# Performance work log

Measured on AMD Instinct MI355X. Metric: run time of the kernel, lower is better.

## Reference

```python
import jax, jax.numpy as jnp
import numpy as np
import math

LIMBS = [(5, 7), (7, 9), (6, 8), (8, 10), (11, 13), (13, 15), (12, 14), (14, 16), (5, 6), (11, 12), (5, 11), (6, 12), (5, 12), (6, 11)]
PARENT = jnp.array([l[0] for l in LIMBS], dtype=jnp.int32)
CHILD = jnp.array([l[1] for l in LIMBS], dtype=jnp.int32)
EXPECTED_2D_LEN = 0.15

B = 65536
D_MODEL = 64
HID = 128


def _ln(x, g, b, eps=1e-5):
    m = jnp.mean(x, axis=-1, keepdims=True)
    v = jnp.mean(jnp.square(x - m), axis=-1, keepdims=True)
    return (x - m) * jax.lax.rsqrt(v + eps) * g + b


def _unit(x, eps=1e-6):
    # F.normalize semantics: divide by max(norm, eps)
    n = jnp.linalg.norm(x, axis=-1, keepdims=True)
    return x / jnp.maximum(n, eps)


def setup_inputs() -> dict:
    key = jax.random.key(0)
    ks = jax.random.split(key, 32)
    d = {}
    d["joint_features"] = jax.random.normal(ks[0], (B, 17, D_MODEL), jnp.float32)
    d["pose_2d"] = jax.random.normal(ks[1], (B, 17, 2), jnp.float32)
    d["pose_3d"] = jax.random.normal(ks[2], (B, 17, 3), jnp.float32)
    d["azimuth"] = jax.random.uniform(ks[3], (B,), jnp.float32) * 360.0
    d["elevation"] = jax.random.uniform(ks[4], (B,), jnp.float32) * 180.0 - 90.0
    d["projected_2d"] = jax.random.normal(ks[5], (B, 17, 2), jnp.float32)

    def lin(k, out_f, in_f, std=None):
        s = std if std is not None else 1.0 / math.sqrt(in_f)
        return jax.random.normal(k, (out_f, in_f), jnp.float32) * s

    # current_orient_encoder: Linear(3->32), LayerNorm(32), ReLU
    d["co_w"] = lin(ks[6], HID // 4, 3)
    d["co_b"] = jnp.zeros((HID // 4,), jnp.float32)
    d["co_g"] = jnp.ones((HID // 4,), jnp.float32)
    d["co_be"] = jnp.zeros((HID // 4,), jnp.float32)
    # limb_2d_encoder: Linear(4->64), LayerNorm(64), ReLU
    d["l2_w"] = lin(ks[7], HID // 2, 4)
    d["l2_b"] = jnp.zeros((HID // 2,), jnp.float32)
    d["l2_g"] = jnp.ones((HID // 2,), jnp.float32)
    d["l2_be"] = jnp.zeros((HID // 2,), jnp.float32)
    # view_encoder: Linear(7->32), ReLU
    d["v_w"] = lin(ks[8], HID // 4, 7)
    d["v_b"] = jnp.zeros((HID // 4,), jnp.float32)
    # limb_head: Linear(256->128), LN(128), LeakyReLU, Linear(128->128), LeakyReLU, Linear(128->3)
    in_dim = HID // 2 + HID // 4 + D_MODEL * 2 + HID // 4  # 256
    d["h1_w"] = lin(ks[9], HID, in_dim)
    d["h1_b"] = jnp.zeros((HID,), jnp.float32)
    d["h_g"] = jnp.ones((HID,), jnp.float32)
    d["h_be"] = jnp.zeros((HID,), jnp.float32)
    d["h2_w"] = lin(ks[10], HID, HID)
    d["h2_b"] = jnp.zeros((HID,), jnp.float32)
    d["h3_w"] = lin(ks[11], 3, HID, std=0.01)
    d["h3_b"] = jnp.zeros((3,), jnp.float32)
    return d


def reference(joint_features, pose_2d, pose_3d, azimuth, elevation, projected_2d,
              co_w, co_b, co_g, co_be, l2_w, l2_b, l2_g, l2_be, v_w, v_b,
              h1_w, h1_b, h_g, h_be, h2_w, h2_b, h3_w, h3_b):
    nl = PARENT.shape[0]  # 14
    # gather parent/child joint features: (B, 14, d_model)
    pf = joint_features[:, PARENT, :]
    cf = joint_features[:, CHILD, :]
    # current 3D orientations from input pose
    cur = _unit(pose_3d[:, CHILD, :] - pose_3d[:, PARENT, :])  # (B,14,3)
    co = jax.nn.relu(_ln(jnp.einsum('blk,ok->blo', cur, co_w) + co_b, co_g, co_be))
    # view encoder from azimuth/elevation
    az = azimuth * (math.pi / 180.0)
    el = elevation * (math.pi / 180.0)
    sa, ca, se, ce = jnp.sin(az), jnp.cos(az), jnp.sin(el), jnp.cos(el)
    view_in = jnp.stack([sa * ce, se, ca * ce, sa, ca, se, ce], axis=-1)  # (B,7)
    vf = jax.nn.relu(view_in @ v_w.T + v_b)  # (B,32)
    vf = jnp.broadcast_to(vf[:, None, :], (vf.shape[0], nl, vf.shape[-1]))
    # 2D foreshortening features from projected_2d
    v2 = projected_2d[:, CHILD, :] - projected_2d[:, PARENT, :]  # (B,14,2)
    L = jnp.linalg.norm(v2, axis=-1, keepdims=True)
    d2 = v2 / (L + 1e-6)
    ratio = L / (EXPECTED_2D_LEN + 1e-6)
    feat2d = jnp.concatenate([d2, L, ratio], axis=-1)  # (B,14,4)
    l2 = jax.nn.relu(_ln(jnp.einsum('blk,ok->blo', feat2d, l2_w) + l2_b, l2_g, l2_be))
    # concat all branches: (B,14,256)
    lf = jnp.concatenate([l2, co, pf, cf, vf], axis=-1)
    # 3-layer MLP head
    h = jax.nn.leaky_relu(_ln(jnp.einsum('blk,ok->blo', lf, h1_w) + h1_b, h_g, h_be), 0.2)
    h = jax.nn.leaky_relu(jnp.einsum('blk,ok->blo', h, h2_w) + h2_b, 0.2)
    delta = jnp.einsum('blk,ok->blo', h, h3_w) + h3_b  # (B,14,3)
    return _unit(cur + delta)
```

## Files before the change

kernel.cpp:

```cpp
#include <hip/hip_runtime.h>


#define NTHR   1024
#define NBLK   256
#define NTILES 14336
#define NROWS  917504
#define C2D    6.66662222251852f
#define RAD    0.017453292519943295f
#define WS_STAT_OFF 98304
#define WS_SCAL_OFF 131072

typedef __bf16 bf16x8 __attribute__((ext_vector_type(8)));
typedef __bf16 bf16x4 __attribute__((ext_vector_type(4)));
typedef float  f32x4  __attribute__((ext_vector_type(4)));

#define PARENT_PK 0x10106097863120ull
#define CHILD_PK  0x677671b9a85342ull

__global__ __launch_bounds__(256) void prep_kernel(
    const float* __restrict__ w1, const float* __restrict__ w2,
    __bf16* __restrict__ wsb)
{
  const int u = blockIdx.x * 256 + threadIdx.x;
  if (u < 4096) {
    const int lane = u & 63, t = u >> 6;
    const int f = t & 1, kk = (t >> 1) & 7, wn = t >> 4;
    const int col = wn * 32 + f * 16 + (lane & 15);
    const int kb  = kk * 32 + (lane >> 4) * 8;
    __bf16* dst = wsb + (size_t)u * 8;
    #pragma unroll
    for (int j = 0; j < 8; ++j) dst[j] = (__bf16)w1[col * 256 + kb + j];
  } else if (u < 6144) {
    const int v = u - 4096;
    const int lane = v & 63, t = v >> 6;
    const int f = t & 1, kk = (t >> 1) & 3, wn = t >> 3;
    const int col = wn * 32 + f * 16 + (lane & 15);
    const int kb  = kk * 32 + (lane >> 4) * 8;
    __bf16* dst = wsb + 32768 + (size_t)v * 8;
    #pragma unroll
    for (int j = 0; j < 8; ++j) dst[j] = (__bf16)w2[col * 128 + kb + j];
  }
}

__global__ __launch_bounds__(64) void prep0_kernel(
    const float* __restrict__ cow, const float* __restrict__ cob,
    const float* __restrict__ l2w, const float* __restrict__ l2b,
    float* __restrict__ statg)
{
  const int o = threadIdx.x;
  const float w0 = l2w[o * 4 + 0], w1v = l2w[o * 4 + 1];
  const float w2v = l2w[o * 4 + 2] + C2D * l2w[o * 4 + 3];
  const float bo = l2b[o];
  float v[14] = { w0, w1v, w2v, bo, w0 * w0, w0 * w1v, w0 * w2v,
                  w1v * w1v, w1v * w2v, w2v * w2v, w0 * bo, w1v * bo, w2v * bo, bo * bo };
  float c0 = 0.f, c1 = 0.f, c2 = 0.f, cb = 0.f;
  if (o < 32) { c0 = cow[o * 3 + 0]; c1 = cow[o * 3 + 1]; c2 = cow[o * 3 + 2]; cb = cob[o]; }
  float u[14] = { c0, c1, c2, cb, c0 * c0, c0 * c1, c0 * c2,
                  c1 * c1, c1 * c2, c2 * c2, c0 * cb, c1 * cb, c2 * cb, cb * cb };
  #pragma unroll
  for (int k = 0; k < 14; ++k) {
    #pragma unroll
    for (int m = 1; m < 64; m <<= 1) { v[k] += __shfl_xor(v[k], m, 64); u[k] += __shfl_xor(u[k], m, 64); }
  }
  if (o == 0) {
    const float i64 = 1.f / 64.f, i32 = 1.f / 32.f;
    const float lmx = v[0] * i64, lmy = v[1] * i64, lmz = v[2] * i64, lmb = v[3] * i64;
    statg[0] = lmx; statg[1] = lmy; statg[2] = lmz; statg[3] = lmb;
    statg[4] = v[4] * i64 - lmx * lmx;        statg[5] = 2.f * (v[5] * i64 - lmx * lmy);
    statg[6] = 2.f * (v[6] * i64 - lmx * lmz); statg[7] = v[7] * i64 - lmy * lmy;
    statg[8] = 2.f * (v[8] * i64 - lmy * lmz); statg[9] = v[9] * i64 - lmz * lmz;
    statg[10] = 2.f * (v[10] * i64 - lmx * lmb); statg[11] = 2.f * (v[11] * i64 - lmy * lmb);
    statg[12] = 2.f * (v[12] * i64 - lmz * lmb); statg[13] = v[13] * i64 - lmb * lmb;
    const float cmx = u[0] * i32, cmy = u[1] * i32, cmz = u[2] * i32, cmb = u[3] * i32;
    statg[14] = cmx; statg[15] = cmy; statg[16] = cmz; statg[17] = cmb;
    statg[18] = u[4] * i32 - cmx * cmx;        statg[19] = 2.f * (u[5] * i32 - cmx * cmy);
    statg[20] = 2.f * (u[6] * i32 - cmx * cmz); statg[21] = u[7] * i32 - cmy * cmy;
    statg[22] = 2.f * (u[8] * i32 - cmy * cmz); statg[23] = u[9] * i32 - cmz * cmz;
    statg[24] = 2.f * (u[10] * i32 - cmx * cmb); statg[25] = 2.f * (u[11] * i32 - cmy * cmb);
    statg[26] = 2.f * (u[12] * i32 - cmz * cmb); statg[27] = u[13] * i32 - cmb * cmb;
  }
}

__global__ __launch_bounds__(256) void prep2_kernel(
    const float* __restrict__ p3g, const float* __restrict__ az,
    const float* __restrict__ el,  const float* __restrict__ p2d,
    const float* __restrict__ statg, f32x4* __restrict__ scalg)
{
  const int r = blockIdx.x * 256 + threadIdx.x;
  const unsigned rg = (unsigned)r;
  const unsigned b = rg / 14u;
  const int l = (int)(rg - b * 14u);
  const int p = 5 + (int)((PARENT_PK >> (4 * l)) & 15ull);
  const int c = 5 + (int)((CHILD_PK  >> (4 * l)) & 15ull);
  const float* p3 = p3g + (size_t)b * 51;
  const float dx = p3[c * 3 + 0] - p3[p * 3 + 0];
  const float dy = p3[c * 3 + 1] - p3[p * 3 + 1];
  const float dz = p3[c * 3 + 2] - p3[p * 3 + 2];
  const float* q2 = p2d + (size_t)b * 34;
  const float vx = q2[c * 2 + 0] - q2[p * 2 + 0];
  const float vy = q2[c * 2 + 1] - q2[p * 2 + 1];
  const float sazv = az[b], selv = el[b];

  const float ci = 1.f / fmaxf(sqrtf(dx * dx + dy * dy + dz * dz), 1e-6f);
  const float cx = dx * ci, cy = dy * ci, cz = dz * ci;
  const float L  = sqrtf(vx * vx + vy * vy);
  const float il = 1.f / (L + 1e-6f);
  const float f0 = vx * il, f1 = vy * il;
  const float azr = sazv * RAD, elr = selv * RAD;
  const float sa = __sinf(azr), ca = __cosf(azr);
  const float se = __sinf(elr), ce = __cosf(elr);
  const float vl = statg[4] * f0 * f0 + statg[7] * f1 * f1 + statg[9] * L * L +
                   statg[5] * f0 * f1 + statg[6] * f0 * L + statg[8] * f1 * L +
                   statg[10] * f0 + statg[11] * f1 + statg[12] * L + statg[13];
  const float vc = statg[18] * cx * cx + statg[21] * cy * cy + statg[23] * cz * cz +
                   statg[19] * cx * cy + statg[20] * cx * cz + statg[22] * cy * cz +
                   statg[24] * cx + statg[25] * cy + statg[26] * cz + statg[27];
  f32x4 s0; s0[0] = cx; s0[1] = cy; s0[2] = cz; s0[3] = f0;
  f32x4 s1; s1[0] = f1; s1[1] = L; s1[2] = rsqrtf(vl + 1e-5f); s1[3] = rsqrtf(vc + 1e-5f);
  f32x4 s2; s2[0] = sa * ce; s2[1] = se; s2[2] = ca * ce; s2[3] = sa;
  f32x4 s3; s3[0] = ca; s3[1] = ce; s3[2] = 0.f; s3[3] = 0.f;
  scalg[(size_t)r * 4 + 0] = s0; scalg[(size_t)r * 4 + 1] = s1;
  scalg[(size_t)r * 4 + 2] = s2; scalg[(size_t)r * 4 + 3] = s3;
}

struct Smem {
  __bf16 w1f[32768];
  __bf16 w2f[16384];
  __bf16 lf[64][264];
  __bf16 h [64][132];
  f32x4  scal4[256];
  float  w3c[384];
  float  h1b[128], hg[128], hbe[128], h2b[128];
  float  partG1[512];
  float  partG2[768];
};

__device__ __forceinline__ float RFL(float x) {
  return __uint_as_float((unsigned)__builtin_amdgcn_readfirstlane((int)__float_as_uint(x)));
}

template<bool PRECOMP>
__global__ __launch_bounds__(NTHR, 4) void limb_kernel(
    const float* __restrict__ jf,  const float* __restrict__ p3g,
    const float* __restrict__ az,  const float* __restrict__ el,
    const float* __restrict__ p2d,
    const float* __restrict__ cow, const float* __restrict__ cob,
    const float* __restrict__ cog, const float* __restrict__ cobe,
    const float* __restrict__ l2w, const float* __restrict__ l2b,
    const float* __restrict__ l2g, const float* __restrict__ l2be,
    const float* __restrict__ vw,  const float* __restrict__ vb,
    const float* __restrict__ h1bg, const float* __restrict__ hgg,
    const float* __restrict__ hbeg, const float* __restrict__ h2bg,
    const float* __restrict__ w3,  const float* __restrict__ h3bg,
    const __bf16* __restrict__ wsb, const f32x4* __restrict__ scalg,
    float* __restrict__ out)
{
  __shared__ Smem sm;
  const int tid  = threadIdx.x;
  const int wave = tid >> 6;
  const int lane = tid & 63;
  const int lrow = lane & 15, lk8 = lane >> 4;
  const int mp = wave >> 2, nt = wave & 3;
  const int nrow = nt * 16 + lrow;
  const int cb0 = mp * 32 + lk8 * 4;
  const int cb1 = cb0 + 16;
  const int myrow0 = wave * 4;

  {
    const uint4* s1 = (const uint4*)wsb;
    uint4* d1 = (uint4*)sm.w1f;
    for (int i = tid; i < 4096; i += NTHR) d1[i] = s1[i];
    const uint4* s2 = (const uint4*)(wsb + 32768);
    uint4* d2 = (uint4*)sm.w2f;
    for (int i = tid; i < 2048; i += NTHR) d2[i] = s2[i];
  }
  if (tid < 384) sm.w3c[tid] = w3[tid];
  if (tid < 128) {
    sm.h1b[tid] = h1bg[tid]; sm.hg[tid] = hgg[tid];
    sm.hbe[tid] = hbeg[tid]; sm.h2b[tid] = h2bg[tid];
  }
  const float h3b0 = h3bg[0], h3b1 = h3bg[1], h3b2 = h3bg[2];

  float lQxx, lQxy2, lQxz2, lQyy, lQyz2, lQzz, lrx2, lry2, lrz2, ls0;
  float lmx, lmy, lmz, lmb;
  {
    float s1x = 0, s1y = 0, s1z = 0, sb = 0;
    float sxx = 0, sxy = 0, sxz = 0, syy = 0, syz = 0, szz = 0;
    float sbx = 0, sby = 0, sbz = 0, sbb = 0;
    for (int o = 0; o < 64; ++o) {
      const float w0 = l2w[o * 4 + 0], w1v = l2w[o * 4 + 1];
      const float w2v = l2w[o * 4 + 2] + C2D * l2w[o * 4 + 3];
      const float bo = l2b[o];
      s1x += w0; s1y += w1v; s1z += w2v; sb += bo;
      sxx += w0 * w0; sxy += w0 * w1v; sxz += w0 * w2v;
      syy += w1v * w1v; syz += w1v * w2v; szz += w2v * w2v;
      sbx += w0 * bo; sby += w1v * bo; sbz += w2v * bo; sbb += bo * bo;
    }
    const float i = 1.f / 64.f;
    lmx = RFL(s1x * i); lmy = RFL(s1y * i); lmz = RFL(s1z * i); lmb = RFL(sb * i);
    lQxx = RFL(sxx * i - lmx * lmx); lQxy2 = RFL(2.f * (sxy * i - lmx * lmy));
    lQxz2 = RFL(2.f * (sxz * i - lmx * lmz)); lQyy = RFL(syy * i - lmy * lmy);
    lQyz2 = RFL(2.f * (syz * i - lmy * lmz)); lQzz = RFL(szz * i - lmz * lmz);
    lrx2 = RFL(2.f * (sbx * i - lmx * lmb)); lry2 = RFL(2.f * (sby * i - lmy * lmb));
    lrz2 = RFL(2.f * (sbz * i - lmz * lmb)); ls0 = RFL(sbb * i - lmb * lmb);
  }
  float cQxx, cQxy2, cQxz2, cQyy, cQyz2, cQzz, crx2, cry2, crz2, cs0;
  float cmx, cmy, cmz, cmb;
  {
    float s1x = 0, s1y = 0, s1z = 0, sb = 0;
    float sxx = 0, sxy = 0, sxz = 0, syy = 0, syz = 0, szz = 0;
    float sbx = 0, sby = 0, sbz = 0, sbb = 0;
    for (int o = 0; o < 32; ++o) {
      const float w0 = cow[o * 3 + 0], w1v = cow[o * 3 + 1], w2v = cow[o * 3 + 2];
      const float bo = cob[o];
      s1x += w0; s1y += w1v; s1z += w2v; sb += bo;
      sxx += w0 * w0; sxy += w0 * w1v; sxz += w0 * w2v;
      syy += w1v * w1v; syz += w1v * w2v; szz += w2v * w2v;
      sbx += w0 * bo; sby += w1v * bo; sbz += w2v * bo; sbb += bo * bo;
    }
    const float i = 1.f / 32.f;
    cmx = RFL(s1x * i); cmy = RFL(s1y * i); cmz = RFL(s1z * i); cmb = RFL(sb * i);
    cQxx = RFL(sxx * i - cmx * cmx); cQxy2 = RFL(2.f * (sxy * i - cmx * cmy));
    cQxz2 = RFL(2.f * (sxz * i - cmx * cmz)); cQyy = RFL(syy * i - cmy * cmy);
    cQyz2 = RFL(2.f * (syz * i - cmy * cmz)); cQzz = RFL(szz * i - cmz * cmz);
    crx2 = RFL(2.f * (sbx * i - cmx * cmb)); cry2 = RFL(2.f * (sby * i - cmy * cmb));
    crz2 = RFL(2.f * (sbz * i - cmz * cmb)); cs0 = RFL(sbb * i - cmb * cmb);
  }

  const float lwc0 = l2w[lane * 4 + 0] - lmx;
  const float lwc1 = l2w[lane * 4 + 1] - lmy;
  const float lwc2 = (l2w[lane * 4 + 2] + C2D * l2w[lane * 4 + 3]) - lmz;
  const float lbc  = l2b[lane] - lmb;
  const float lgv  = l2g[lane], lbev = l2be[lane];
  float u0, u1, u2, u3, u4, u5, u6;
  if (lane < 32) {
    u0 = cow[lane * 3 + 0] - cmx; u1 = cow[lane * 3 + 1] - cmy;
    u2 = cow[lane * 3 + 2] - cmz; u3 = cob[lane] - cmb;
    u4 = cog[lane]; u5 = cobe[lane]; u6 = 0.f;
  } else {
    const int o = lane - 32;
    u0 = vw[o * 7 + 0]; u1 = vw[o * 7 + 1] + vw[o * 7 + 5];
    u2 = vw[o * 7 + 2]; u3 = vw[o * 7 + 3];
    u4 = vw[o * 7 + 4]; u5 = vw[o * 7 + 6]; u6 = vb[o];
  }

  auto jf_src = [&](int rg0x, int round) -> const float* {
    const int task = wave * 8 + round * 4 + lk8;
    const int row = task >> 1, half = task & 1;
    const unsigned rg = (unsigned)(rg0x + row);
    const unsigned b = rg / 14u;
    const int l = (int)(rg - b * 14u);
    const int j = half ? 5 + (int)((CHILD_PK >> (4 * l)) & 15ull)
                       : 5 + (int)((PARENT_PK >> (4 * l)) & 15ull);
    return jf + ((size_t)b * 17 + (size_t)j) * 64 + lrow * 4;
  };
  auto jf_store = [&](int round, float4 v) {
    const int task = wave * 8 + round * 4 + lk8;
    const int row = task >> 1, half = task & 1;
    bf16x4 o; o[0] = (__bf16)v.x; o[1] = (__bf16)v.y; o[2] = (__bf16)v.z; o[3] = (__bf16)v.w;
    *(bf16x4*)&sm.lf[row][(half ? 160 : 96) + lrow * 4] = o;
  };
  struct G12 { float p3p0, p3p1, p3p2, p3c0, p3c1, p3c2, q2p0, q2p1, q2c0, q2c1, sazv, selv; };
  auto gather12_row = [&](int rgl) -> G12 {
    G12 g;
    const unsigned rg = (unsigned)rgl;
    const unsigned b = rg / 14u;
    const int l = (int)(rg - b * 14u);
    const int p = 5 + (int)((PARENT_PK >> (4 * l)) & 15ull);
    const int c = 5 + (int)((CHILD_PK  >> (4 * l)) & 15ull);
    const float* p3 = p3g + (size_t)b * 51;
    g.p3p0 = p3[p * 3 + 0]; g.p3p1 = p3[p * 3 + 1]; g.p3p2 = p3[p * 3 + 2];
    g.p3c0 = p3[c * 3 + 0]; g.p3c1 = p3[c * 3 + 1]; g.p3c2 = p3[c * 3 + 2];
    const float* q2 = p2d + (size_t)b * 34;
    g.q2p0 = q2[p * 2 + 0]; g.q2p1 = q2[p * 2 + 1];
    g.q2c0 = q2[c * 2 + 0]; g.q2c1 = q2[c * 2 + 1];
    g.sazv = az[b]; g.selv = el[b];
    return g;
  };
  auto scal_write = [&](int row, const G12& g) {
    const float dx = g.p3c0 - g.p3p0, dy = g.p3c1 - g.p3p1, dz = g.p3c2 - g.p3p2;
    const float ci = 1.f / fmaxf(sqrtf(dx * dx + dy * dy + dz * dz), 1e-6f);
    const float cx = dx * ci, cy = dy * ci, cz = dz * ci;
    const float vx = g.q2c0 - g.q2p0, vy = g.q2c1 - g.q2p1;
    const float L  = sqrtf(vx * vx + vy * vy);
    const float il = 1.f / (L + 1e-6f);
    const float f0 = vx * il, f1 = vy * il;
    const float azr = g.sazv * RAD, elr = g.selv * RAD;
    const float sa = __sinf(azr), ca = __cosf(azr);
    const float se = __sinf(elr), ce = __cosf(elr);
    const float vl = lQxx * f0 * f0 + lQyy * f1 * f1 + lQzz * L * L +
                     lQxy2 * f0 * f1 + lQxz2 * f0 * L + lQyz2 * f1 * L +
                     lrx2 * f0 + lry2 * f1 + lrz2 * L + ls0;
    const float vc = cQxx * cx * cx + cQyy * cy * cy + cQzz * cz * cz +
                     cQxy2 * cx * cy + cQxz2 * cx * cz + cQyz2 * cy * cz +
                     crx2 * cx + cry2 * cy + crz2 * cz + cs0;
    f32x4 s0; s0[0] = cx; s0[1] = cy; s0[2] = cz; s0[3] = f0;
    f32x4 s1; s1[0] = f1; s1[1] = L; s1[2] = rsqrtf(vl + 1e-5f); s1[3] = rsqrtf(vc + 1e-5f);
    f32x4 s2; s2[0] = sa * ce; s2[1] = se; s2[2] = ca * ce; s2[3] = sa;
    f32x4 s3; s3[0] = ca; s3[1] = ce; s3[2] = 0.f; s3[3] = 0.f;
    sm.scal4[row * 4 + 0] = s0; sm.scal4[row * 4 + 1] = s1;
    sm.scal4[row * 4 + 2] = s2; sm.scal4[row * 4 + 3] = s3;
  };
  auto expandB = [&]() {
    #pragma unroll
    for (int rr = 0; rr < 4; ++rr) {
      const int row = myrow0 + rr;
      const f32x4 s0 = sm.scal4[row * 4 + 0];
      const f32x4 s1 = sm.scal4[row * 4 + 1];
      const f32x4 s2 = sm.scal4[row * 4 + 2];
      const f32x4 s3 = sm.scal4[row * 4 + 3];
      {
        const float a = lwc0 * s0[3] + lwc1 * s1[0] + lwc2 * s1[1] + lbc;
        sm.lf[row][lane] = (__bf16)fmaxf(a * s1[2] * lgv + lbev, 0.f);
      }
      if (lane < 32) {
        const float a = u0 * s0[0] + u1 * s0[1] + u2 * s0[2] + u3;
        sm.lf[row][64 + lane] = (__bf16)fmaxf(a * s1[3] * u4 + u5, 0.f);
      } else {
        const float a = u0 * s2[0] + u1 * s2[1] + u2 * s2[2] + u3 * s2[3] +
                        u4 * s3[0] + u5 * s3[1] + u6;
        sm.lf[row][224 + (lane - 32)] = (__bf16)fmaxf(a, 0.f);
      }
    }
  };

  {
    const int rg0 = blockIdx.x * 64;
    jf_store(0, *(const float4*)jf_src(rg0, 0));
    jf_store(1, *(const float4*)jf_src(rg0, 1));
    if (PRECOMP) {
      if (lane < 16)
        sm.scal4[(myrow0 + (lane >> 2)) * 4 + (lane & 3)] =
            scalg[(size_t)(rg0 + myrow0 + (lane >> 2)) * 4 + (lane & 3)];
    } else if (lane < 4) {
      scal_write(myrow0 + lane, gather12_row(rg0 + myrow0 + lane));
    }
    expandB();
  }
  __syncthreads();

  float curx = 0.f, cury = 0.f, curz = 0.f;
  int prevT = -1;

  for (int tile = blockIdx.x; tile < NTILES; tile += NBLK) {
    const int ntile = tile + NBLK;
    const bool pv = ntile < NTILES;

    float4 jva = {0.f, 0.f, 0.f, 0.f}, jvb = jva;
    f32x4 sn = {0.f, 0.f, 0.f, 0.f};
    G12 g = {};
    if (pv) {
      jva = *(const float4*)jf_src(ntile * 64, 0);
      jvb = *(const float4*)jf_src(ntile * 64, 1);
      if (PRECOMP) {
        if (lane < 16)
          sn = scalg[(size_t)(ntile * 64 + myrow0 + (lane >> 2)) * 4 + (lane & 3)];
      } else if (lane < 4) {
        g = gather12_row(ntile * 64 + myrow0 + lane);
      }
    }
    if (prevT >= 0 && lane < 4) {
      const int r = myrow0 + lane;
      const f32x4 q0 = *(const f32x4*)&sm.partG2[r * 12];
      const f32x4 q1 = *(const f32x4*)&sm.partG2[r * 12 + 4];
      const f32x4 q2 = *(const f32x4*)&sm.partG2[r * 12 + 8];
      const float ox = curx + q0[0] + q0[1] + q0[2] + q0[3] + h3b0;
      const float oy = cury + q1[0] + q1[1] + q1[2] + q1[3] + h3b1;
      const float oz = curz + q2[0] + q2[1] + q2[2] + q2[3] + h3b2;
      const float nn = sqrtf(ox * ox + oy * oy + oz * oz);
      const float iv = 1.f / fmaxf(nn, 1e-6f);
      const size_t o0 = (size_t)(prevT * 64 + r) * 3;
      out[o0 + 0] = ox * iv; out[o0 + 1] = oy * iv; out[o0 + 2] = oz * iv;
    }
    f32x4 a0 = {0.f, 0.f, 0.f, 0.f}, a1 = a0;
    #pragma unroll
    for (int kk = 0; kk < 8; ++kk) {
      const bf16x8 fb  = *(const bf16x8*)&sm.lf[nrow][kk * 32 + lk8 * 8];
      const bf16x8 fa0 = *(const bf16x8*)&sm.w1f[(((mp * 8 + kk) * 2 + 0) * 64 + lane) * 8];
      const bf16x8 fa1 = *(const bf16x8*)&sm.w1f[(((mp * 8 + kk) * 2 + 1) * 64 + lane) * 8];
      a0 = __builtin_amdgcn_mfma_f32_16x16x32_bf16(fa0, fb, a0, 0, 0, 0);
      a1 = __builtin_amdgcn_mfma_f32_16x16x32_bf16(fa1, fb, a1, 0, 0, 0);
    }
    const f32x4 hb0 = *(const f32x4*)&sm.h1b[cb0];
    const f32x4 hb1 = *(const f32x4*)&sm.h1b[cb1];
    float v0[4], v1[4], ss = 0.f, qq = 0.f;
    #pragma unroll
    for (int j = 0; j < 4; ++j) {
      v0[j] = a0[j] + hb0[j]; v1[j] = a1[j] + hb1[j];
      ss += v0[j] + v1[j];
      qq = fmaf(v0[j], v0[j], qq); qq = fmaf(v1[j], v1[j], qq);
    }
    ss += __shfl_xor(ss, 16, 64); ss += __shfl_xor(ss, 32, 64);
    qq += __shfl_xor(qq, 16, 64); qq += __shfl_xor(qq, 32, 64);
    if (lk8 == 0) *(float2*)&sm.partG1[nrow * 8 + mp * 2] = make_float2(ss, qq);
    __syncthreads();

    {
      const f32x4 pa = *(const f32x4*)&sm.partG1[nrow * 8];
      const f32x4 pb = *(const f32x4*)&sm.partG1[nrow * 8 + 4];
      const float mean = (pa[0] + pa[2] + pb[0] + pb[2]) * (1.f / 128.f);
      const float var  = (pa[1] + pa[3] + pb[1] + pb[3]) * (1.f / 128.f) - mean * mean;
      const float rs = rsqrtf(var + 1e-5f);
      const f32x4 g0 = *(const f32x4*)&sm.hg[cb0],  g1 = *(const f32x4*)&sm.hg[cb1];
      const f32x4 e0 = *(const f32x4*)&sm.hbe[cb0], e1 = *(const f32x4*)&sm.hbe[cb1];
      bf16x4 y0, y1;
      #pragma unroll
      for (int j = 0; j < 4; ++j) {
        float t0 = (v0[j] - mean) * rs * g0[j] + e0[j]; t0 = (t0 > 0.f) ? t0 : 0.2f * t0;
        float t1 = (v1[j] - mean) * rs * g1[j] + e1[j]; t1 = (t1 > 0.f) ? t1 : 0.2f * t1;
        y0[j] = (__bf16)t0; y1[j] = (__bf16)t1;
      }
      *(bf16x4*)&sm.h[nrow][cb0] = y0;
      *(bf16x4*)&sm.h[nrow][cb1] = y1;
    }
    __syncthreads();

    f32x4 d0 = {0.f, 0.f, 0.f, 0.f}, d1 = d0;
    #pragma unroll
    for (int kk = 0; kk < 4; ++kk) {
      const bf16x8 fbh = *(const bf16x8*)&sm.h[nrow][kk * 32 + lk8 * 8];
      const bf16x8 fa0 = *(const bf16x8*)&sm.w2f[(((mp * 4 + kk) * 2 + 0) * 64 + lane) * 8];
      const bf16x8 fa1 = *(const bf16x8*)&sm.w2f[(((mp * 4 + kk) * 2 + 1) * 64 + lane) * 8];
      d0 = __builtin_amdgcn_mfma_f32_16x16x32_bf16(fa0, fbh, d0, 0, 0, 0);
      d1 = __builtin_amdgcn_mfma_f32_16x16x32_bf16(fa1, fbh, d1, 0, 0, 0);
    }
    if (pv) { jf_store(0, jva); jf_store(1, jvb); }
    if (lane < 4) {
      const f32x4 cu = sm.scal4[(myrow0 + lane) * 4];
      curx = cu[0]; cury = cu[1]; curz = cu[2];
    }
    if (pv) {
      if (PRECOMP) {
        if (lane < 16)
          sm.scal4[(myrow0 + (lane >> 2)) * 4 + (lane & 3)] = sn;
      } else if (lane < 4) {
        scal_write(myrow0 + lane, g);
      }
    }
    {
      const f32x4 b20 = *(const f32x4*)&sm.h2b[cb0], b21 = *(const f32x4*)&sm.h2b[cb1];
      const f32x4 wx0 = *(const f32x4*)&sm.w3c[cb0],        wx1 = *(const f32x4*)&sm.w3c[cb1];
      const f32x4 wy0 = *(const f32x4*)&sm.w3c[128 + cb0],  wy1 = *(const f32x4*)&sm.w3c[128 + cb1];
      const f32x4 wz0 = *(const f32x4*)&sm.w3c[256 + cb0],  wz1 = *(const f32x4*)&sm.w3c[256 + cb1];
      float p0 = 0.f, p1 = 0.f, p2 = 0.f;
      #pragma unroll
      for (int j = 0; j < 4; ++j) {
        float x0 = d0[j] + b20[j]; x0 = (x0 > 0.f) ? x0 : 0.2f * x0;
        float x1 = d1[j] + b21[j]; x1 = (x1 > 0.f) ? x1 : 0.2f * x1;
        p0 = fmaf(x0, wx0[j], fmaf(x1, wx1[j], p0));
        p1 = fmaf(x0, wy0[j], fmaf(x1, wy1[j], p1));
        p2 = fmaf(x0, wz0[j], fmaf(x1, wz1[j], p2));
      }
      p0 += __shfl_xor(p0, 16, 64); p0 += __shfl_xor(p0, 32, 64);
      p1 += __shfl_xor(p1, 16, 64); p1 += __shfl_xor(p1, 32, 64);
      p2 += __shfl_xor(p2, 16, 64); p2 += __shfl_xor(p2, 32, 64);
      if (lk8 == 0) {
        sm.partG2[nrow * 12 + 0 + mp] = p0;
        sm.partG2[nrow * 12 + 4 + mp] = p1;
        sm.partG2[nrow * 12 + 8 + mp] = p2;
      }
    }
    if (pv) expandB();
    __syncthreads();
    prevT = tile;
  }

  if (lane < 4) {
    const int r = myrow0 + lane;
    const f32x4 q0 = *(const f32x4*)&sm.partG2[r * 12];
    const f32x4 q1 = *(const f32x4*)&sm.partG2[r * 12 + 4];
    const f32x4 q2 = *(const f32x4*)&sm.partG2[r * 12 + 8];
    const float ox = curx + q0[0] + q0[1] + q0[2] + q0[3] + h3b0;
    const float oy = cury + q1[0] + q1[1] + q1[2] + q1[3] + h3b1;
    const float oz = curz + q2[0] + q2[1] + q2[2] + q2[3] + h3b2;
    const float nn = sqrtf(ox * ox + oy * oy + oz * oz);
    const float iv = 1.f / fmaxf(nn, 1e-6f);
    const size_t o0 = (size_t)(prevT * 64 + r) * 3;
    out[o0 + 0] = ox * iv; out[o0 + 1] = oy * iv; out[o0 + 2] = oz * iv;
  }
}

extern "C" void kernel_launch(void* const* d_in, const int* in_sizes, int n_in,
                              void* d_out, int out_size, void* d_ws, size_t ws_size,
                              hipStream_t stream) {
  (void)in_sizes; (void)n_in; (void)out_size;
  const float* jf   = (const float*)d_in[0];
  const float* p3   = (const float*)d_in[2];
  const float* az   = (const float*)d_in[3];
  const float* el   = (const float*)d_in[4];
  const float* p2d  = (const float*)d_in[5];
  const float* cow  = (const float*)d_in[6];
  const float* cob  = (const float*)d_in[7];
  const float* cog  = (const float*)d_in[8];
  const float* cobe = (const float*)d_in[9];
  const float* l2w  = (const float*)d_in[10];
  const float* l2b  = (const float*)d_in[11];
  const float* l2g  = (const float*)d_in[12];
  const float* l2be = (const float*)d_in[13];
  const float* vw   = (const float*)d_in[14];
  const float* vb   = (const float*)d_in[15];
  const float* w1   = (const float*)d_in[16];
  const float* h1b  = (const float*)d_in[17];
  const float* hg   = (const float*)d_in[18];
  const float* hbe  = (const float*)d_in[19];
  const float* w2   = (const float*)d_in[20];
  const float* h2b  = (const float*)d_in[21];
  const float* w3   = (const float*)d_in[22];
  const float* h3b  = (const float*)d_in[23];

  __bf16* wsb   = (__bf16*)d_ws;
  float*  statg = (float*)((char*)d_ws + WS_STAT_OFF);
  f32x4*  scalg = (f32x4*)((char*)d_ws + WS_SCAL_OFF);

  const size_t ws_need = (size_t)WS_SCAL_OFF + (size_t)NROWS * 64;
  const bool pre = ws_size >= ws_need;

  prep_kernel<<<dim3(24), dim3(256), 0, stream>>>(w1, w2, wsb);
  if (pre) {
    prep0_kernel<<<dim3(1), dim3(64), 0, stream>>>(cow, cob, l2w, l2b, statg);
    prep2_kernel<<<dim3(NROWS / 256), dim3(256), 0, stream>>>(p3, az, el, p2d, statg, scalg);
    limb_kernel<true><<<dim3(NBLK), dim3(NTHR), 0, stream>>>(
        jf, p3, az, el, p2d, cow, cob, cog, cobe,
        l2w, l2b, l2g, l2be, vw, vb,
        h1b, hg, hbe, h2b, w3, h3b, wsb, scalg, (float*)d_out);
  } else {
    limb_kernel<false><<<dim3(NBLK), dim3(NTHR), 0, stream>>>(
        jf, p3, az, el, p2d, cow, cob, cog, cobe,
        l2w, l2b, l2g, l2be, vw, vb,
        h1b, hg, hbe, h2b, w3, h3b, wsb, scalg, (float*)d_out);
  }
}
```

Before: 292.1 us.

## Compute small encoder branches with an MFMA over precomputed bf16 scalar features

The prep kernel now folds the LayerNorm statistics, gains and biases of the limb_2d, orientation and view encoders into a single 16-wide bf16 weight matrix. Each row's scalars are written as a 16-element bf16 feature vector plus a separate fp32 current-orientation buffer, instead of 64 bytes of fp32 scalars. In the main kernel the per-lane scalar expansion is replaced by two 16x16x32 MFMAs per wave. The lf concat layout and w1 columns are permuted so these branches occupy contiguous columns 0-127. This cuts per-row global traffic and VALU work in the expansion, at the cost of bf16 rounding of the normalized pre-activations and an extra barrier in the prologue.

```diff
diff --git a/kernel.cpp b/kernel.cpp
--- a/kernel.cpp
+++ b/kernel.cpp
@@ -7,8 +7,10 @@
 #define NROWS  917504
 #define C2D    6.66662222251852f
 #define RAD    0.017453292519943295f
-#define WS_STAT_OFF 98304
-#define WS_SCAL_OFF 131072
+#define WS_WSM_OFF  98304
+#define WS_STAT_OFF 106496
+#define WS_X_OFF    131072
+#define WS_CUR_OFF  (131072 + 29360128)
 
 typedef __bf16 bf16x8 __attribute__((ext_vector_type(8)));
 typedef __bf16 bf16x4 __attribute__((ext_vector_type(4)));
@@ -29,7 +31,11 @@
     const int kb  = kk * 32 + (lane >> 4) * 8;
     __bf16* dst = wsb + (size_t)u * 8;
     #pragma unroll
-    for (int j = 0; j < 8; ++j) dst[j] = (__bf16)w1[col * 256 + kb + j];
+    for (int j = 0; j < 8; ++j) {
+      const int kn = kb + j;
+      const int ko = kn < 96 ? kn : (kn < 128 ? kn + 128 : kn - 32);
+      dst[j] = (__bf16)w1[col * 256 + ko];
+    }
   } else if (u < 6144) {
     const int v = u - 4096;
     const int lane = v & 63, t = v >> 6;
@@ -42,19 +48,23 @@
   }
 }
 
-__global__ __launch_bounds__(64) void prep0_kernel(
+__global__ __launch_bounds__(128) void prep0_kernel(
     const float* __restrict__ cow, const float* __restrict__ cob,
+    const float* __restrict__ cog, const float* __restrict__ cobe,
     const float* __restrict__ l2w, const float* __restrict__ l2b,
-    float* __restrict__ statg)
+    const float* __restrict__ l2g, const float* __restrict__ l2be,
+    const float* __restrict__ vw,  const float* __restrict__ vb,
+    float* __restrict__ statg, __bf16* __restrict__ wsmg)
 {
-  const int o = threadIdx.x;
-  const float w0 = l2w[o * 4 + 0], w1v = l2w[o * 4 + 1];
-  const float w2v = l2w[o * 4 + 2] + C2D * l2w[o * 4 + 3];
-  const float bo = l2b[o];
+  const int tid = threadIdx.x;
+  const int o64 = tid & 63;
+  const float w0 = l2w[o64 * 4 + 0], w1v = l2w[o64 * 4 + 1];
+  const float w2v = l2w[o64 * 4 + 2] + C2D * l2w[o64 * 4 + 3];
+  const float bo = l2b[o64];
   float v[14] = { w0, w1v, w2v, bo, w0 * w0, w0 * w1v, w0 * w2v,
                   w1v * w1v, w1v * w2v, w2v * w2v, w0 * bo, w1v * bo, w2v * bo, bo * bo };
   float c0 = 0.f, c1 = 0.f, c2 = 0.f, cb = 0.f;
-  if (o < 32) { c0 = cow[o * 3 + 0]; c1 = cow[o * 3 + 1]; c2 = cow[o * 3 + 2]; cb = cob[o]; }
+  if (o64 < 32) { c0 = cow[o64 * 3 + 0]; c1 = cow[o64 * 3 + 1]; c2 = cow[o64 * 3 + 2]; cb = cob[o64]; }
   float u[14] = { c0, c1, c2, cb, c0 * c0, c0 * c1, c0 * c2,
                   c1 * c1, c1 * c2, c2 * c2, c0 * cb, c1 * cb, c2 * cb, cb * cb };
   #pragma unroll
@@ -62,16 +72,16 @@
     #pragma unroll
     for (int m = 1; m < 64; m <<= 1) { v[k] += __shfl_xor(v[k], m, 64); u[k] += __shfl_xor(u[k], m, 64); }
   }
-  if (o == 0) {
-    const float i64 = 1.f / 64.f, i32 = 1.f / 32.f;
-    const float lmx = v[0] * i64, lmy = v[1] * i64, lmz = v[2] * i64, lmb = v[3] * i64;
+  const float i64 = 1.f / 64.f, i32 = 1.f / 32.f;
+  const float lmx = v[0] * i64, lmy = v[1] * i64, lmz = v[2] * i64, lmb = v[3] * i64;
+  const float cmx = u[0] * i32, cmy = u[1] * i32, cmz = u[2] * i32, cmb = u[3] * i32;
+  if (tid == 0) {
     statg[0] = lmx; statg[1] = lmy; statg[2] = lmz; statg[3] = lmb;
     statg[4] = v[4] * i64 - lmx * lmx;        statg[5] = 2.f * (v[5] * i64 - lmx * lmy);
     statg[6] = 2.f * (v[6] * i64 - lmx * lmz); statg[7] = v[7] * i64 - lmy * lmy;
     statg[8] = 2.f * (v[8] * i64 - lmy * lmz); statg[9] = v[9] * i64 - lmz * lmz;
     statg[10] = 2.f * (v[10] * i64 - lmx * lmb); statg[11] = 2.f * (v[11] * i64 - lmy * lmb);
     statg[12] = 2.f * (v[12] * i64 - lmz * lmb); statg[13] = v[13] * i64 - lmb * lmb;
-    const float cmx = u[0] * i32, cmy = u[1] * i32, cmz = u[2] * i32, cmb = u[3] * i32;
     statg[14] = cmx; statg[15] = cmy; statg[16] = cmz; statg[17] = cmb;
     statg[18] = u[4] * i32 - cmx * cmx;        statg[19] = 2.f * (u[5] * i32 - cmx * cmy);
     statg[20] = 2.f * (u[6] * i32 - cmx * cmz); statg[21] = u[7] * i32 - cmy * cmy;
@@ -79,12 +89,52 @@
     statg[24] = 2.f * (u[10] * i32 - cmx * cmb); statg[25] = 2.f * (u[11] * i32 - cmy * cmb);
     statg[26] = 2.f * (u[12] * i32 - cmz * cmb); statg[27] = u[13] * i32 - cmb * cmb;
   }
+  float W[16];
+  #pragma unroll
+  for (int k = 0; k < 16; ++k) W[k] = 0.f;
+  const int col = tid;
+  if (col < 64) {
+    const float g = l2g[col], be = l2be[col];
+    W[0] = g * (l2w[col * 4 + 0] - lmx);
+    W[1] = g * (l2w[col * 4 + 1] - lmy);
+    W[2] = g * ((l2w[col * 4 + 2] + C2D * l2w[col * 4 + 3]) - lmz);
+    W[3] = g * (l2b[col] - lmb);
+    W[14] = be;
+  } else if (col < 96) {
+    const int o = col - 64;
+    const float g = cog[o], be = cobe[o];
+    W[4] = g * (cow[o * 3 + 0] - cmx);
+    W[5] = g * (cow[o * 3 + 1] - cmy);
+    W[6] = g * (cow[o * 3 + 2] - cmz);
+    W[7] = g * (cob[o] - cmb);
+    W[14] = be;
+  } else {
+    const int o = col - 96;
+    W[8]  = vw[o * 7 + 0];
+    W[9]  = vw[o * 7 + 1] + vw[o * 7 + 5];
+    W[10] = vw[o * 7 + 2];
+    W[11] = vw[o * 7 + 3];
+    W[12] = vw[o * 7 + 4];
+    W[13] = vw[o * 7 + 6];
+    W[14] = vb[o];
+  }
+  const int mp = col >> 5, f = (col >> 4) & 1, lcol = col & 15;
+  #pragma unroll
+  for (int kq = 0; kq < 4; ++kq) {
+    #pragma unroll
+    for (int j = 0; j < 8; ++j) {
+      const int k = kq * 8 + j;
+      wsmg[(size_t)(((mp * 2 + f) * 64 + kq * 16 + lcol)) * 8 + j] =
+          (__bf16)(k < 16 ? W[k] : 0.f);
+    }
+  }
 }
 
 __global__ __launch_bounds__(256) void prep2_kernel(
     const float* __restrict__ p3g, const float* __restrict__ az,
     const float* __restrict__ el,  const float* __restrict__ p2d,
-    const float* __restrict__ statg, f32x4* __restrict__ scalg)
+    const float* __restrict__ statg, __bf16* __restrict__ Xg,
+    f32x4* __restrict__ curg)
 {
   const int r = blockIdx.x * 256 + threadIdx.x;
   const unsigned rg = (unsigned)r;
@@ -115,12 +165,23 @@
   const float vc = statg[18] * cx * cx + statg[21] * cy * cy + statg[23] * cz * cz +
                    statg[19] * cx * cy + statg[20] * cx * cz + statg[22] * cy * cz +
                    statg[24] * cx + statg[25] * cy + statg[26] * cz + statg[27];
-  f32x4 s0; s0[0] = cx; s0[1] = cy; s0[2] = cz; s0[3] = f0;
-  f32x4 s1; s1[0] = f1; s1[1] = L; s1[2] = rsqrtf(vl + 1e-5f); s1[3] = rsqrtf(vc + 1e-5f);
-  f32x4 s2; s2[0] = sa * ce; s2[1] = se; s2[2] = ca * ce; s2[3] = sa;
-  f32x4 s3; s3[0] = ca; s3[1] = ce; s3[2] = 0.f; s3[3] = 0.f;
-  scalg[(size_t)r * 4 + 0] = s0; scalg[(size_t)r * 4 + 1] = s1;
-  scalg[(size_t)r * 4 + 2] = s2; scalg[(size_t)r * 4 + 3] = s3;
+  const float rs2 = rsqrtf(vl + 1e-5f);
+  const float rsc = rsqrtf(vc + 1e-5f);
+
+  __bf16 xr[16];
+  xr[0] = (__bf16)(f0 * rs2);  xr[1] = (__bf16)(f1 * rs2);
+  xr[2] = (__bf16)(L * rs2);   xr[3] = (__bf16)rs2;
+  xr[4] = (__bf16)(cx * rsc);  xr[5] = (__bf16)(cy * rsc);
+  xr[6] = (__bf16)(cz * rsc);  xr[7] = (__bf16)rsc;
+  xr[8] = (__bf16)(sa * ce);   xr[9] = (__bf16)se;
+  xr[10] = (__bf16)(ca * ce);  xr[11] = (__bf16)sa;
+  xr[12] = (__bf16)ca;         xr[13] = (__bf16)ce;
+  xr[14] = (__bf16)1.0f;       xr[15] = (__bf16)0.0f;
+  uint4* xd = (uint4*)(Xg + (size_t)r * 16);
+  xd[0] = *(const uint4*)&xr[0];
+  xd[1] = *(const uint4*)&xr[8];
+  f32x4 cu; cu[0] = cx; cu[1] = cy; cu[2] = cz; cu[3] = 0.f;
+  curg[r] = cu;
 }
 
 struct Smem {
@@ -128,7 +189,7 @@
   __bf16 w2f[16384];
   __bf16 lf[64][264];
   __bf16 h [64][132];
-  f32x4  scal4[256];
+  __bf16 X [64][40];
   float  w3c[384];
   float  h1b[128], hg[128], hbe[128], h2b[128];
   float  partG1[512];
@@ -152,7 +213,8 @@
     const float* __restrict__ h1bg, const float* __restrict__ hgg,
     const float* __restrict__ hbeg, const float* __restrict__ h2bg,
     const float* __restrict__ w3,  const float* __restrict__ h3bg,
-    const __bf16* __restrict__ wsb, const f32x4* __restrict__ scalg,
+    const __bf16* __restrict__ wsb, const __bf16* __restrict__ Xg,
+    const f32x4* __restrict__ curg,
     float* __restrict__ out)
 {
   __shared__ Smem sm;
@@ -166,6 +228,8 @@
   const int cb1 = cb0 + 16;
   const int myrow0 = wave * 4;
 
+  const bf16x8* __restrict__ wsm8 = (const bf16x8*)(wsb + 49152);
+
   {
     const uint4* s1 = (const uint4*)wsb;
     uint4* d1 = (uint4*)sm.w1f;
@@ -174,6 +238,7 @@
     uint4* d2 = (uint4*)sm.w2f;
     for (int i = tid; i < 2048; i += NTHR) d2[i] = s2[i];
   }
+  for (int i = tid; i < 64 * 40; i += NTHR) ((__bf16*)sm.X)[i] = (__bf16)0.0f;
   if (tid < 384) sm.w3c[tid] = w3[tid];
   if (tid < 128) {
     sm.h1b[tid] = h1bg[tid]; sm.hg[tid] = hgg[tid];
@@ -244,6 +309,8 @@
     u4 = vw[o * 7 + 4]; u5 = vw[o * 7 + 6]; u6 = vb[o];
   }
 
+  f32x4* const scal4u = (f32x4*)&sm.X[0][0];
+
   auto jf_src = [&](int rg0x, int round) -> const float* {
     const int task = wave * 8 + round * 4 + lk8;
     const int row = task >> 1, half = task & 1;
@@ -258,7 +325,7 @@
     const int task = wave * 8 + round * 4 + lk8;
     const int row = task >> 1, half = task & 1;
     bf16x4 o; o[0] = (__bf16)v.x; o[1] = (__bf16)v.y; o[2] = (__bf16)v.z; o[3] = (__bf16)v.w;
-    *(bf16x4*)&sm.lf[row][(half ? 160 : 96) + lrow * 4] = o;
+    *(bf16x4*)&sm.lf[row][(half ? 192 : 128) + lrow * 4] = o;
   };
   struct G12 { float p3p0, p3p1, p3p2, p3c0, p3c1, p3c2, q2p0, q2p1, q2c0, q2c1, sazv, selv; };
   auto gather12_row = [&](int rgl) -> G12 {
@@ -298,17 +365,17 @@
     f32x4 s1; s1[0] = f1; s1[1] = L; s1[2] = rsqrtf(vl + 1e-5f); s1[3] = rsqrtf(vc + 1e-5f);
     f32x4 s2; s2[0] = sa * ce; s2[1] = se; s2[2] = ca * ce; s2[3] = sa;
     f32x4 s3; s3[0] = ca; s3[1] = ce; s3[2] = 0.f; s3[3] = 0.f;
-    sm.scal4[row * 4 + 0] = s0; sm.scal4[row * 4 + 1] = s1;
-    sm.scal4[row * 4 + 2] = s2; sm.scal4[row * 4 + 3] = s3;
+    scal4u[row * 4 + 0] = s0; scal4u[row * 4 + 1] = s1;
+    scal4u[row * 4 + 2] = s2; scal4u[row * 4 + 3] = s3;
   };
   auto expandB = [&]() {
     #pragma unroll
     for (int rr = 0; rr < 4; ++rr) {
       const int row = myrow0 + rr;
-      const f32x4 s0 = sm.scal4[row * 4 + 0];
-      const f32x4 s1 = sm.scal4[row * 4 + 1];
-      const f32x4 s2 = sm.scal4[row * 4 + 2];
-      const f32x4 s3 = sm.scal4[row * 4 + 3];
+      const f32x4 s0 = scal4u[row * 4 + 0];
+      const f32x4 s1 = scal4u[row * 4 + 1];
+      const f32x4 s2 = scal4u[row * 4 + 2];
+      const f32x4 s3 = scal4u[row * 4 + 3];
       {
         const float a = lwc0 * s0[3] + lwc1 * s1[0] + lwc2 * s1[1] + lbc;
         sm.lf[row][lane] = (__bf16)fmaxf(a * s1[2] * lgv + lbev, 0.f);
@@ -319,9 +386,25 @@
       } else {
         const float a = u0 * s2[0] + u1 * s2[1] + u2 * s2[2] + u3 * s2[3] +
                         u4 * s3[0] + u5 * s3[1] + u6;
-        sm.lf[row][224 + (lane - 32)] = (__bf16)fmaxf(a, 0.f);
-      }
-    }
+        sm.lf[row][96 + (lane - 32)] = (__bf16)fmaxf(a, 0.f);
+      }
+    }
+  };
+  auto expandMFMA = [&]() {
+    const bf16x8 fbX = *(const bf16x8*)&sm.X[nrow][lk8 * 8];
+    const bf16x8 wa0 = wsm8[(mp * 2 + 0) * 64 + lane];
+    const bf16x8 wa1 = wsm8[(mp * 2 + 1) * 64 + lane];
+    f32x4 e0 = {0.f, 0.f, 0.f, 0.f}, e1 = e0;
+    e0 = __builtin_amdgcn_mfma_f32_16x16x32_bf16(wa0, fbX, e0, 0, 0, 0);
+    e1 = __builtin_amdgcn_mfma_f32_16x16x32_bf16(wa1, fbX, e1, 0, 0, 0);
+    bf16x4 y0, y1;
+    #pragma unroll
+    for (int j = 0; j < 4; ++j) {
+      y0[j] = (__bf16)fmaxf(e0[j], 0.f);
+      y1[j] = (__bf16)fmaxf(e1[j], 0.f);
+    }
+    *(bf16x4*)&sm.lf[nrow][cb0] = y0;
+    *(bf16x4*)&sm.lf[nrow][cb1] = y1;
   };
 
   {
@@ -329,13 +412,16 @@
     jf_store(0, *(const float4*)jf_src(rg0, 0));
     jf_store(1, *(const float4*)jf_src(rg0, 1));
     if (PRECOMP) {
-      if (lane < 16)
-        sm.scal4[(myrow0 + (lane >> 2)) * 4 + (lane & 3)] =
-            scalg[(size_t)(rg0 + myrow0 + (lane >> 2)) * 4 + (lane & 3)];
+      if (lane < 8) {
+        const int row = myrow0 + (lane >> 1), ch = lane & 1;
+        *(uint4*)&sm.X[row][ch * 8] =
+            ((const uint4*)(Xg + (size_t)(rg0 + row) * 16))[ch];
+      }
     } else if (lane < 4) {
       scal_write(myrow0 + lane, gather12_row(rg0 + myrow0 + lane));
     }
-    expandB();
+    __syncthreads();
+    if (PRECOMP) expandMFMA(); else expandB();
   }
   __syncthreads();
 
@@ -347,14 +433,18 @@
     const bool pv = ntile < NTILES;
 
     float4 jva = {0.f, 0.f, 0.f, 0.f}, jvb = jva;
-    f32x4 sn = {0.f, 0.f, 0.f, 0.f};
+    uint4 xv = {0, 0, 0, 0};
+    f32x4 cn = {0.f, 0.f, 0.f, 0.f};
     G12 g = {};
+    if (PRECOMP && lane < 4) cn = curg[(size_t)tile * 64 + myrow0 + lane];
     if (pv) {
       jva = *(const float4*)jf_src(ntile * 64, 0);
       jvb = *(const float4*)jf_src(ntile * 64, 1);
       if (PRECOMP) {
-        if (lane < 16)
-          sn = scalg[(size_t)(ntile * 64 + myrow0 + (lane >> 2)) * 4 + (lane & 3)];
+        if (lane < 8) {
+          const int row = myrow0 + (lane >> 1), ch = lane & 1;
+          xv = ((const uint4*)(Xg + (size_t)(ntile * 64 + row) * 16))[ch];
+        }
       } else if (lane < 4) {
         g = gather12_row(ntile * 64 + myrow0 + lane);
       }
@@ -413,6 +503,10 @@
       *(bf16x4*)&sm.h[nrow][cb0] = y0;
       *(bf16x4*)&sm.h[nrow][cb1] = y1;
     }
+    if (PRECOMP && pv && lane < 8) {
+      const int row = myrow0 + (lane >> 1), ch = lane & 1;
+      *(uint4*)&sm.X[row][ch * 8] = xv;
+    }
     __syncthreads();
 
     f32x4 d0 = {0.f, 0.f, 0.f, 0.f}, d1 = d0;
@@ -426,15 +520,12 @@
     }
     if (pv) { jf_store(0, jva); jf_store(1, jvb); }
     if (lane < 4) {
-      const f32x4 cu = sm.scal4[(myrow0 + lane) * 4];
-      curx = cu[0]; cury = cu[1]; curz = cu[2];
-    }
-    if (pv) {
       if (PRECOMP) {
-        if (lane < 16)
-          sm.scal4[(myrow0 + (lane >> 2)) * 4 + (lane & 3)] = sn;
-      } else if (lane < 4) {
-        scal_write(myrow0 + lane, g);
+        curx = cn[0]; cury = cn[1]; curz = cn[2];
+      } else {
+        const f32x4 cu = scal4u[(myrow0 + lane) * 4];
+        curx = cu[0]; cury = cu[1]; curz = cu[2];
+        if (pv) scal_write(myrow0 + lane, g);
       }
     }
     {
@@ -460,7 +551,7 @@
         sm.partG2[nrow * 12 + 8 + mp] = p2;
       }
     }
-    if (pv) expandB();
+    if (pv) { if (PRECOMP) expandMFMA(); else expandB(); }
     __syncthreads();
     prevT = tile;
   }
@@ -509,24 +600,29 @@
   const float* h3b  = (const float*)d_in[23];
 
   __bf16* wsb   = (__bf16*)d_ws;
+  __bf16* wsmg  = (__bf16*)((char*)d_ws + WS_WSM_OFF);
   float*  statg = (float*)((char*)d_ws + WS_STAT_OFF);
-  f32x4*  scalg = (f32x4*)((char*)d_ws + WS_SCAL_OFF);
-
-  const size_t ws_need = (size_t)WS_SCAL_OFF + (size_t)NROWS * 64;
+  __bf16* Xg    = (__bf16*)((char*)d_ws + WS_X_OFF);
+  f32x4*  curg  = (f32x4*)((char*)d_ws + WS_CUR_OFF);
+
+  const size_t ws_need = (size_t)WS_CUR_OFF + (size_t)NROWS * 16;
   const bool pre = ws_size >= ws_need;
 
   prep_kernel<<<dim3(24), dim3(256), 0, stream>>>(w1, w2, wsb);
   if (pre) {
-    prep0_kernel<<<dim3(1), dim3(64), 0, stream>>>(cow, cob, l2w, l2b, statg);
-    prep2_kernel<<<dim3(NROWS / 256), dim3(256), 0, stream>>>(p3, az, el, p2d, statg, scalg);
+    prep0_kernel<<<dim3(1), dim3(128), 0, stream>>>(cow, cob, cog, cobe,
+                                                    l2w, l2b, l2g, l2be, vw, vb,
+                                                    statg, wsmg);
+    prep2_kernel<<<dim3(NROWS / 256), dim3(256), 0, stream>>>(p3, az, el, p2d,
+                                                              statg, Xg, curg);
     limb_kernel<true><<<dim3(NBLK), dim3(NTHR), 0, stream>>>(
         jf, p3, az, el, p2d, cow, cob, cog, cobe,
         l2w, l2b, l2g, l2be, vw, vb,
-        h1b, hg, hbe, h2b, w3, h3b, wsb, scalg, (float*)d_out);
+        h1b, hg, hbe, h2b, w3, h3b, wsb, Xg, curg, (float*)d_out);
   } else {
     limb_kernel<false><<<dim3(NBLK), dim3(NTHR), 0, stream>>>(
         jf, p3, az, el, p2d, cow, cob, cog, cobe,
         l2w, l2b, l2g, l2be, vw, vb,
-        h1b, hg, hbe, h2b, w3, h3b, wsb, scalg, (float*)d_out);
+        h1b, hg, hbe, h2b, w3, h3b, wsb, Xg, curg, (float*)d_out);
   }
 }
```

Measured after the change: 668.5 us. +128.8%, slower.
